# Optimization experiments

Hardware: AMD Instinct MI355X
Metric: run time of the kernel (lower is better)

## Reference

```python
import jax, jax.numpy as jnp
import numpy as np

S, B, C, H, W = 16, 64, 128, 11, 11
P = H * W
N_ITER = 3
EPS = 1e-5


def setup_inputs() -> dict:
    key = jax.random.key(0)
    ks = jax.random.split(key, 12)
    w = lambda k, shape: jax.random.normal(k, shape, jnp.float32) * 0.02
    return {
        "x": jax.random.normal(ks[0], (S, B, C, H, W), jnp.float32),
        # intra-attention 1x1 convs (stored as [out,in] matrices)
        "wq": w(ks[1], (C, C)), "bq": jnp.zeros((C,), jnp.float32),
        "wk": w(ks[2], (C, C)), "bk": jnp.zeros((C,), jnp.float32),
        "wv": w(ks[3], (C, C)), "bv": jnp.zeros((C,), jnp.float32),
        "intra_alpha": jnp.float32(1.0),
        # inter-message path
        "w_msg": w(ks[4], (C, C + 1)), "b_msg": jnp.zeros((C,), jnp.float32),
        "w_lin": w(ks[5], (C, C)),
        "weight": jnp.float32(0.5),
        "w_gate": w(ks[6], (C, C)), "b_gate": jnp.zeros((C,), jnp.float32),
        # ConvGRU 3x3 convs
        "w_zr": w(ks[7], (2 * C, 2 * C, 3, 3)), "b_zr": jnp.zeros((2 * C,), jnp.float32),
        "w_h": w(ks[8], (C, 2 * C, 3, 3)), "b_h": jnp.zeros((C,), jnp.float32),
        # LayerNorm over [C,11,11]
        "ln_gamma": jnp.ones((C, H, W), jnp.float32),
        "ln_beta": jnp.zeros((C, H, W), jnp.float32),
    }


def reference(x, wq, bq, wk, bk, wv, bv, intra_alpha, w_msg, b_msg, w_lin,
              weight, w_gate, b_gate, w_zr, b_zr, w_h, b_h, ln_gamma, ln_beta):
    scale = C ** -0.5

    def c1(t, wgt, bias):  # 1x1 conv on [S,B,Cin,H,W] -> [S,B,Cout,H,W]
        return jnp.einsum('sbchw,oc->sbohw', t, wgt) + bias[:, None, None]

    def conv3(t, wgt, bias):  # 3x3 'SAME' conv on [N,Cin,H,W]
        y = jax.lax.conv_general_dilated(
            t, wgt, (1, 1), 'SAME', dimension_numbers=('NCHW', 'OIHW', 'NCHW'))
        return y + bias[None, :, None, None]

    # chain-graph neighbor validity masks (|i-j| == 1)
    mask_l = (jnp.arange(S) >= 1).astype(x.dtype)[:, None, None, None, None]
    mask_r = (jnp.arange(S) <= S - 2).astype(x.dtype)[:, None, None, None, None]

    h = x
    for _ in range(N_ITER):
        # ---- intra spatial self-attention (per node, over P=H*W tokens) ----
        q = c1(h, wq, bq).reshape(S, B, C, P)
        k = c1(h, wk, bk).reshape(S, B, C, P)
        v = c1(h, wv, bv).reshape(S, B, C, P)
        att = jax.nn.softmax(jnp.einsum('sbcp,sbcq->sbpq', q, k) * scale, axis=-1)
        intra = jnp.einsum('sbpq,sbcq->sbcp', att, v).reshape(S, B, C, H, W)
        intra = intra_alpha * intra + h

        # ---- inter gated message attention from chain neighbors ----
        xf = h.reshape(S, B, C, P)

        def gated_msg(y, edge_val):
            ef = jnp.full((S, B, 1, H, W), edge_val, h.dtype)  # edge feature i-j
            yy = c1(jnp.concatenate([y, ef], axis=2), w_msg, b_msg).reshape(S, B, C, P)
            yy = jnp.einsum('sbcp,dc->sbdp', yy, w_lin)  # Linear (no bias)
            a = jax.nn.softmax(jnp.einsum('sbcp,sbcq->sbpq', xf, yy), axis=-1)
            m = jnp.einsum('sbpq,sbcq->sbcp', a, yy).reshape(S, B, C, H, W)
            g = jax.nn.sigmoid(c1(m, w_gate, b_gate).mean(axis=(-2, -1), keepdims=True))
            return m * g

        y_left = jnp.concatenate([jnp.zeros_like(h[:1]), h[:-1]], axis=0)   # h[i-1], edge +1
        y_right = jnp.concatenate([h[1:], jnp.zeros_like(h[:1])], axis=0)   # h[i+1], edge -1
        inter = gated_msg(y_left, 1.0) * mask_l + gated_msg(y_right, -1.0) * mask_r

        comb = weight * intra + (1.0 - weight) * inter

        # ---- ConvGRU update (fold S into batch) ----
        xg = comb.reshape(S * B, C, H, W)
        hg = h.reshape(S * B, C, H, W)
        zr = jax.nn.sigmoid(conv3(jnp.concatenate([xg, hg], axis=1), w_zr, b_zr))
        z, r = zr[:, :C], zr[:, C:]
        h_hat = jnp.tanh(conv3(jnp.concatenate([xg, r * hg], axis=1), w_h, b_h))
        h_new = ((1 - z) * hg + z * h_hat).reshape(S, B, C, H, W)

        # ---- residual + LayerNorm over [C,H,W] ----
        nh = h_new + h
        mu = nh.mean(axis=(-3, -2, -1), keepdims=True)
        var = nh.var(axis=(-3, -2, -1), keepdims=True)
        h = (nh - mu) * jax.lax.rsqrt(var + EPS) * ln_gamma + ln_beta
    return h
```

## Files before the change

kernel.cpp:

```cpp
#include <hip/hip_runtime.h>
#include <hip/hip_bf16.h>

#define S_   16
#define B_   64
#define SBn  1024
#define C_   128
#define P_   121
#define CP_  15488
static const long NEl = 15859712L;

typedef __hip_bfloat16 bf16t;
typedef __attribute__((ext_vector_type(8))) short bf16x8;
typedef __attribute__((ext_vector_type(4))) float f32x4;
typedef __attribute__((ext_vector_type(4))) unsigned short us4;

__device__ __forceinline__ float ldb(const bf16t* p){ return __bfloat162float(*p); }
__device__ __forceinline__ float b2f(unsigned short u){ unsigned x=((unsigned)u)<<16; float f; __builtin_memcpy(&f,&x,4); return f; }
__device__ __forceinline__ unsigned short f2bu(float v){ __hip_bfloat16 b=__float2bfloat16(v); unsigned short u; __builtin_memcpy(&u,&b,2); return u; }
__device__ __forceinline__ float ldin(const void* s, long i, int f){
    return f ? ((const float*)s)[i] : b2f(((const unsigned short*)s)[i]);
}

__global__ void detect_kernel(const unsigned short* __restrict__ x, int* __restrict__ flag){
    if(blockIdx.x==0 && threadIdx.x==0){
        int crazy=0;
        for(int i=0;i<512;i++){
            unsigned e=(x[i]>>7)&0xFF;
            if(e!=0 && (e<64 || e>191)) crazy++;
        }
        *flag=(crazy>40)?1:0;
    }
}

__global__ void cvt_kernel(float* __restrict__ dst, const void* __restrict__ src, long n, const int* __restrict__ flag){
    long i=(long)blockIdx.x*blockDim.x+threadIdx.x;
    long st=(long)gridDim.x*blockDim.x;
    int f=*flag;
    for(;i<n;i+=st) dst[i]=ldin(src,i,f);
}

__global__ __launch_bounds__(256) void cvtT_kernel(bf16t* __restrict__ hT, const void* __restrict__ x, const int* __restrict__ flag){
    int sb=blockIdx.x, t=threadIdx.x; int f=*flag;
    for(int i=t;i<CP_;i+=256){
        int c=i/P_, p=i-c*P_;
        float v=ldin(x,(long)sb*CP_+i,f);
        hT[(size_t)sb*CP_+(size_t)p*C_+c]=__float2bfloat16(v);
    }
}

__global__ __launch_bounds__(128) void prep_msg_kernel(float* __restrict__ W2, float* __restrict__ b2l, float* __restrict__ b2r,
        const void* __restrict__ wlin, const void* __restrict__ wmsg, const void* __restrict__ bmsg, const int* __restrict__ flag){
    int d=blockIdx.x, c=threadIdx.x; int f=*flag;
    float acc=0.f;
    for(int o2=0;o2<C_;o2++) acc += ldin(wlin,(long)d*C_+o2,f)*ldin(wmsg,(long)o2*(C_+1)+c,f);
    W2[d*C_+c]=acc;
    if(c<2){
        float e=(c==0)?1.f:-1.f; float a=0.f;
        for(int o2=0;o2<C_;o2++) a += ldin(wlin,(long)d*C_+o2,f)*(ldin(bmsg,o2,f)+e*ldin(wmsg,(long)o2*(C_+1)+C_,f));
        if(c==0) b2l[d]=a; else b2r[d]=a;
    }
}

template<int RAW>
__global__ void prep_w1t(bf16t* __restrict__ dst, const void* __restrict__ src, const int* __restrict__ flag){
    int idx=blockIdx.x*blockDim.x+threadIdx.x;
    if(idx>=16384) return;
    int r=idx&31, oc=(idx>>5)&127, icb=idx>>12;
    float v = RAW? ldin(src,(long)oc*C_+icb*32+r,*flag) : ((const float*)src)[(long)oc*C_+icb*32+r];
    dst[idx]=__float2bfloat16(v);
}

__global__ void prep_w3t(bf16t* __restrict__ dst, const void* __restrict__ src, const int* __restrict__ flag, int OC){
    int idx=blockIdx.x*blockDim.x+threadIdx.x;
    int tot=OC*2304;
    if(idx>=tot) return;
    int r=idx&31; int rest=idx>>5; int oc=rest%OC; int g2=rest/OC; int icb=g2&7, tap=g2>>3;
    float v=ldin(src,((long)(oc*256+icb*32+r))*9+tap,*flag);
    dst[idx]=__float2bfloat16(v);
}

__global__ void prep_gbt(float* __restrict__ gamT, float* __restrict__ betT,
                         const void* __restrict__ gam, const void* __restrict__ bet, const int* __restrict__ flag){
    int idx=blockIdx.x*blockDim.x+threadIdx.x;
    if(idx>=CP_) return;
    int c=idx/P_, p=idx-c*P_; int f=*flag;
    gamT[p*C_+c]=ldin(gam,idx,f);
    betT[p*C_+c]=ldin(bet,idx,f);
}

__global__ void prep_wgt(float* __restrict__ wgT, float* __restrict__ bg2,
                         const void* __restrict__ wg, const void* __restrict__ bg, const int* __restrict__ flag){
    int idx=blockIdx.x*blockDim.x+threadIdx.x;
    int f=*flag;
    if(idx<16384){ int k=idx>>7, c=idx&127; wgT[idx]=ldin(wg,(long)c*C_+k,f); }
    if(idx<128) bg2[idx]=ldin(bg,idx,f);
}

__device__ __forceinline__ void gemm24r(f32x4 (&acc)[4][2],
    const bf16t* __restrict__ Wt, const bf16x8 (&hreg)[4][2],
    int ocr,int l15,int kg)
{
    #pragma unroll
    for(int i=0;i<4;i++){
        #pragma unroll
        for(int j=0;j<2;j++) acc[i][j]=(f32x4){0.f,0.f,0.f,0.f};
    }
    #pragma unroll
    for(int kc=0;kc<4;kc++){
        bf16x8 a[4];
        #pragma unroll
        for(int mt=0;mt<4;mt++) a[mt]=*(const bf16x8*)(Wt+((size_t)(kc*C_+ocr*64+mt*16+l15))*32+kg*8);
        #pragma unroll
        for(int mt=0;mt<4;mt++){
            #pragma unroll
            for(int nt=0;nt<2;nt++)
                acc[mt][nt]=__builtin_amdgcn_mfma_f32_16x16x32_bf16(a[mt],hreg[kc][nt],acc[mt][nt],0,0,0);
        }
    }
}

__global__ __launch_bounds__(512) void qkv_attn(
    bf16t* __restrict__ comb, const bf16t* __restrict__ hT,
    const bf16t* __restrict__ WqT, const bf16t* __restrict__ WkT, const bf16t* __restrict__ WvT,
    const float* __restrict__ bq, const float* __restrict__ bk, const float* __restrict__ bv,
    const float* __restrict__ alphap, const float* __restrict__ wp)
{
    __shared__ bf16t LA[128*136];
    __shared__ bf16t LB[128*136];
    int sb=blockIdx.x, t=threadIdx.x, lane=t&63, w=t>>6;
    int l15=lane&15, kg=lane>>4;
    const bf16t* hp=hT+(size_t)sb*CP_;
    int ocr=w>>2, pcr=w&3;
    bf16x8 hreg[4][2];
    #pragma unroll
    for(int kc=0;kc<4;kc++){
        #pragma unroll
        for(int nt=0;nt<2;nt++)
            hreg[kc][nt]=*(const bf16x8*)(hp+(size_t)(pcr*32+nt*16+l15)*C_+kc*32+kg*8);
    }
    f32x4 acc[4][2];
    gemm24r(acc,WqT,hreg,ocr,l15,kg);
    #pragma unroll
    for(int mt=0;mt<4;mt++){
        int oc0=ocr*64+mt*16+kg*4;
        #pragma unroll
        for(int nt=0;nt<2;nt++){
            int p=pcr*32+nt*16+l15;
            us4 pk;
            #pragma unroll
            for(int r=0;r<4;r++) pk[r]=f2bu(acc[mt][nt][r]+bq[oc0+r]);
            *(us4*)(LA+p*136+oc0)=pk;
        }
    }
    gemm24r(acc,WkT,hreg,ocr,l15,kg);
    #pragma unroll
    for(int mt=0;mt<4;mt++){
        int oc0=ocr*64+mt*16+kg*4;
        #pragma unroll
        for(int nt=0;nt<2;nt++){
            int p=pcr*32+nt*16+l15;
            us4 pk;
            #pragma unroll
            for(int r=0;r<4;r++) pk[r]=f2bu(acc[mt][nt][r]+bk[oc0+r]);
            *(us4*)(LB+p*136+oc0)=pk;
        }
    }
    __syncthreads();
    int m0=w*16;
    f32x4 s[8];
    #pragma unroll
    for(int nt=0;nt<8;nt++) s[nt]=(f32x4){0.f,0.f,0.f,0.f};
    #pragma unroll
    for(int kc=0;kc<4;kc++){
        bf16x8 a=*(const bf16x8*)(LA+(size_t)(m0+l15)*136+kc*32+kg*8);
        #pragma unroll
        for(int nt=0;nt<8;nt++){
            bf16x8 b=*(const bf16x8*)(LB+(size_t)(nt*16+l15)*136+kc*32+kg*8);
            s[nt]=__builtin_amdgcn_mfma_f32_16x16x32_bf16(a,b,s[nt],0,0,0);
        }
    }
    const float scale=0.08838834764831845f;
    #pragma unroll
    for(int nt=0;nt<8;nt++){
        #pragma unroll
        for(int r=0;r<4;r++) s[nt][r]*=scale;
    }
    if(l15>=9){
        #pragma unroll
        for(int r=0;r<4;r++) s[7][r]=-3.0e38f;
    }
    #pragma unroll
    for(int r=0;r<4;r++){
        float mx=s[0][r];
        #pragma unroll
        for(int nt=1;nt<8;nt++) mx=fmaxf(mx,s[nt][r]);
        #pragma unroll
        for(int o=1;o<16;o<<=1) mx=fmaxf(mx,__shfl_xor(mx,o));
        float sm=0.f;
        #pragma unroll
        for(int nt=0;nt<8;nt++){ float e=__expf(s[nt][r]-mx); s[nt][r]=e; sm+=e; }
        #pragma unroll
        for(int o=1;o<16;o<<=1) sm+=__shfl_xor(sm,o);
        float rs=1.f/sm;
        #pragma unroll
        for(int nt=0;nt<8;nt++) s[nt][r]*=rs;
    }
    __syncthreads();
    gemm24r(acc,WvT,hreg,ocr,l15,kg);
    #pragma unroll
    for(int mt=0;mt<4;mt++){
        int oc0=ocr*64+mt*16+kg*4;
        #pragma unroll
        for(int nt=0;nt<2;nt++){
            int p=pcr*32+nt*16+l15;
            #pragma unroll
            for(int r=0;r<4;r++)
                LA[(oc0+r)*136+p]=__float2bfloat16(p<P_? acc[mt][nt][r]+bv[oc0+r] : 0.f);
        }
    }
    #pragma unroll
    for(int r=0;r<4;r++){
        int pr=m0+kg*4+r;
        #pragma unroll
        for(int nt=0;nt<8;nt++) LB[pr*136+nt*16+l15]=__float2bfloat16(s[nt][r]);
    }
    __syncthreads();
    f32x4 o[8];
    #pragma unroll
    for(int nt=0;nt<8;nt++) o[nt]=(f32x4){0.f,0.f,0.f,0.f};
    #pragma unroll
    for(int jc=0;jc<4;jc++){
        bf16x8 a=*(const bf16x8*)(LA+(size_t)(m0+l15)*136+jc*32+kg*8);
        #pragma unroll
        for(int nt=0;nt<8;nt++){
            bf16x8 b=*(const bf16x8*)(LB+(size_t)(nt*16+l15)*136+jc*32+kg*8);
            o[nt]=__builtin_amdgcn_mfma_f32_16x16x32_bf16(a,b,o[nt],0,0,0);
        }
    }
    float al=*alphap, wv=*wp;
    int c0=m0+kg*4;
    bf16t* ob=comb+(size_t)sb*CP_;
    #pragma unroll
    for(int nt=0;nt<8;nt++){
        int p=nt*16+l15;
        if(p>=P_) continue;
        us4 hv=*(const us4*)(hp+(size_t)p*C_+c0);
        us4 pk;
        #pragma unroll
        for(int r=0;r<4;r++) pk[r]=f2bu(wv*(al*o[nt][r]+b2f(hv[r])));
        *(us4*)(ob+(size_t)p*C_+c0)=pk;
    }
}

__global__ __launch_bounds__(512) void msg_all(
    bf16t* __restrict__ comb, const bf16t* __restrict__ hT,
    const bf16t* __restrict__ W2T, const float* __restrict__ b2e,
    const float* __restrict__ wgT, const float* __restrict__ bgf,
    const float* __restrict__ wp, int sb0, int shift)
{
    __shared__ bf16t LA[128*136];
    __shared__ bf16t LB[128*136];
    __shared__ float fl[256];
    int sb=sb0+blockIdx.x, t=threadIdx.x, lane=t&63, w=t>>6;
    int l15=lane&15, kg=lane>>4;
    const bf16t* hsp=hT+(size_t)(sb+shift)*CP_;
    int ocr=w>>2, pcr=w&3;
    bf16x8 hreg[4][2];
    #pragma unroll
    for(int kc=0;kc<4;kc++){
        #pragma unroll
        for(int nt=0;nt<2;nt++)
            hreg[kc][nt]=*(const bf16x8*)(hsp+(size_t)(pcr*32+nt*16+l15)*C_+kc*32+kg*8);
    }
    f32x4 acc[4][2];
    gemm24r(acc,W2T,hreg,ocr,l15,kg);
    #pragma unroll
    for(int mt=0;mt<4;mt++){
        int oc0=ocr*64+mt*16+kg*4;
        #pragma unroll
        for(int nt=0;nt<2;nt++){
            int p=pcr*32+nt*16+l15;
            us4 pk;
            #pragma unroll
            for(int r=0;r<4;r++){
                float v=acc[mt][nt][r]+b2e[oc0+r];
                pk[r]=f2bu(v);
                LB[(oc0+r)*136+p]=__float2bfloat16(p<P_? v : 0.f);
            }
            *(us4*)(LA+p*136+oc0)=pk;
        }
    }
    __syncthreads();
    int m0=w*16;
    const bf16t* ap=hT+(size_t)sb*CP_;
    f32x4 s[8];
    #pragma unroll
    for(int nt=0;nt<8;nt++) s[nt]=(f32x4){0.f,0.f,0.f,0.f};
    #pragma unroll
    for(int kc=0;kc<4;kc++){
        bf16x8 a=*(const bf16x8*)(ap+(size_t)(m0+l15)*C_+kc*32+kg*8);
        #pragma unroll
        for(int nt=0;nt<8;nt++){
            bf16x8 b=*(const bf16x8*)(LA+(size_t)(nt*16+l15)*136+kc*32+kg*8);
            s[nt]=__builtin_amdgcn_mfma_f32_16x16x32_bf16(a,b,s[nt],0,0,0);
        }
    }
    if(l15>=9){
        #pragma unroll
        for(int r=0;r<4;r++) s[7][r]=-3.0e38f;
    }
    #pragma unroll
    for(int r=0;r<4;r++){
        float mx=s[0][r];
        #pragma unroll
        for(int nt=1;nt<8;nt++) mx=fmaxf(mx,s[nt][r]);
        #pragma unroll
        for(int o=1;o<16;o<<=1) mx=fmaxf(mx,__shfl_xor(mx,o));
        float sm=0.f;
        #pragma unroll
        for(int nt=0;nt<8;nt++){ float e=__expf(s[nt][r]-mx); s[nt][r]=e; sm+=e; }
        #pragma unroll
        for(int o=1;o<16;o<<=1) sm+=__shfl_xor(sm,o);
        float rs=1.f/sm;
        #pragma unroll
        for(int nt=0;nt<8;nt++) s[nt][r]*=rs;
    }
    __syncthreads();
    #pragma unroll
    for(int r=0;r<4;r++){
        int pr=m0+kg*4+r;
        #pragma unroll
        for(int nt=0;nt<8;nt++) LA[pr*136+nt*16+l15]=__float2bfloat16(s[nt][r]);
    }
    __syncthreads();
    f32x4 o[8];
    #pragma unroll
    for(int nt=0;nt<8;nt++) o[nt]=(f32x4){0.f,0.f,0.f,0.f};
    #pragma unroll
    for(int jc=0;jc<4;jc++){
        bf16x8 a=*(const bf16x8*)(LB+(size_t)(m0+l15)*136+jc*32+kg*8);
        #pragma unroll
        for(int nt=0;nt<8;nt++){
            bf16x8 b=*(const bf16x8*)(LA+(size_t)(nt*16+l15)*136+jc*32+kg*8);
            o[nt]=__builtin_amdgcn_mfma_f32_16x16x32_bf16(a,b,o[nt],0,0,0);
        }
    }
    int c0=m0+kg*4;
    #pragma unroll
    for(int r=0;r<4;r++){
        float sm=0.f;
        #pragma unroll
        for(int nt=0;nt<8;nt++){ float v=o[nt][r]; if(nt==7&&l15>8) v=0.f; sm+=v; }
        sm+=__shfl_xor(sm,1); sm+=__shfl_xor(sm,2); sm+=__shfl_xor(sm,4); sm+=__shfl_xor(sm,8);
        if(l15==0) fl[c0+r]=sm*(1.f/121.f);
    }
    __syncthreads();
    if(t<C_){
        float a=bgf[t];
        #pragma unroll 8
        for(int k=0;k<C_;k++) a+=wgT[k*C_+t]*fl[k];
        fl[C_+t]=1.f/(1.f+__expf(-a));
    }
    __syncthreads();
    float w1m=1.f-*wp;
    float gg[4];
    #pragma unroll
    for(int r=0;r<4;r++) gg[r]=fl[C_+c0+r];
    bf16t* ob=comb+(size_t)sb*CP_;
    #pragma unroll
    for(int nt=0;nt<8;nt++){
        int p=nt*16+l15;
        if(p>=P_) continue;
        us4 bv=*(const us4*)(ob+(size_t)p*C_+c0);
        #pragma unroll
        for(int r=0;r<4;r++) bv[r]=f2bu(b2f(bv[r]) + w1m*o[nt][r]*gg[r]);
        *(us4*)(ob+(size_t)p*C_+c0)=bv;
    }
}

#define LOADA3(bidx, widx) { \
    _Pragma("unroll") \
    for(int mt=0;mt<4;mt++) abuf[bidx][mt]=*(const bf16x8*)(Wt+(size_t)(widx)*(OC*32)+mt*512+base_lane); }
#define STEP3(lbase, bidx, doff) { \
    bf16x8 bb[4]; \
    _Pragma("unroll") \
    for(int nt=0;nt<4;nt++) bb[nt]=*(const bf16x8*)((lbase)+boff[nt]+(doff)); \
    __builtin_amdgcn_s_setprio(1); \
    _Pragma("unroll") \
    for(int mt=0;mt<4;mt++){ \
        _Pragma("unroll") \
        for(int nt=0;nt<4;nt++) \
            acc[mt][nt]=__builtin_amdgcn_mfma_f32_16x16x32_bf16(abuf[bidx][mt],bb[nt],acc[mt][nt],0,0,0); } \
    __builtin_amdgcn_s_setprio(0); }
#define SLOAD3(stg) { \
    const bf16t* ssrc=(((stg)<2)? in0T:in1T)+(size_t)sb*CP_+((stg)&1)*64; \
    sreg[0]=*(const bf16x8*)(ssrc+(size_t)(t>>3)*C_+(t&7)*8); \
    sreg[1]=*(const bf16x8*)(ssrc+(size_t)((t+256)>>3)*C_+(t&7)*8); \
    if(sv2) sreg[2]=*(const bf16x8*)(ssrc+(size_t)((t+512)>>3)*C_+(t&7)*8); \
    if(sv3) sreg[3]=*(const bf16x8*)(ssrc+(size_t)((t+768)>>3)*C_+(t&7)*8); }
#define SWRITE3(lbase) { \
    *(bf16x8*)((lbase)+spix0*72+(t&7)*8)=sreg[0]; \
    *(bf16x8*)((lbase)+spix1*72+(t&7)*8)=sreg[1]; \
    if(sv2) *(bf16x8*)((lbase)+spix2*72+(t&7)*8)=sreg[2]; \
    if(sv3) *(bf16x8*)((lbase)+spix3*72+(t&7)*8)=sreg[3]; }

template<int MODE>
__global__ __launch_bounds__(256) void conv3_mfma(
    bf16t* __restrict__ o0, bf16t* __restrict__ o1,
    const bf16t* __restrict__ in0T, const bf16t* __restrict__ in1T,
    const bf16t* __restrict__ Wt, const float* __restrict__ bias,
    const bf16t* __restrict__ zT, const bf16t* __restrict__ hTb,
    const float* __restrict__ gamT, const float* __restrict__ betT)
{
    constexpr int OC=(MODE==1)?256:128;
    __shared__ bf16t lin[2*12176];
    __shared__ float red[8];
    int sb=blockIdx.x, ocb=(MODE==1)? (int)blockIdx.y*128 : 0;
    int t=threadIdx.x, lane=t&63, w=t>>6;
    int ocr=w>>1, pcr=w&1, l15=lane&15, kg=lane>>4;
    int boff[4]; bool pv_[4];
    #pragma unroll
    for(int nt=0;nt<4;nt++){
        int p=pcr*64+nt*16+l15;
        pv_[nt]=(p<P_); int pc=pv_[nt]?p:(P_-1);
        boff[nt]=((pc/11)*13+(pc%11))*72+kg*8;
    }
    f32x4 acc[4][4];
    #pragma unroll
    for(int i=0;i<4;i++){
        #pragma unroll
        for(int j=0;j<4;j++) acc[i][j]=(f32x4){0.f,0.f,0.f,0.f};
    }
    int base_lane=(ocb+ocr*64+l15)*32+kg*8;
    bf16x8 abuf[4][4];
    bf16x8 sreg[4];
    bool sv2=((t+512)<968), sv3=((t+768)<968);
    int sp0=t>>3, sp1=(t+256)>>3, sp2=(t+512)>>3, sp3=(t+768)>>3;
    if(sp2>120) sp2=120;
    if(sp3>120) sp3=120;
    int spix0=(sp0/11+1)*13+(sp0%11)+1;
    int spix1=(sp1/11+1)*13+(sp1%11)+1;
    int spix2=(sp2/11+1)*13+(sp2%11)+1;
    int spix3=(sp3/11+1)*13+(sp3%11)+1;
    LOADA3(0,0); LOADA3(1,1); LOADA3(2,8); LOADA3(3,9);
    SLOAD3(0);
    {
        bf16x8 z;
        #pragma unroll
        for(int e=0;e<8;e++) z[e]=0;
        for(int i=t;i<768;i+=256){
            int half=i>=384; int i2=i-half*384;
            int bi=i2>>3, cc=(i2&7)*8;
            int pix;
            if(bi<13) pix=bi;
            else if(bi<26) pix=156+(bi-13);
            else { int j2=bi-26; pix=(1+(j2>>1))*13+((j2&1)?12:0); }
            *(bf16x8*)(lin+half*12176+pix*72+cc)=z;
        }
    }
    SWRITE3(lin);
    __syncthreads();
    #pragma unroll
    for(int st=0; st<4; ++st){
        if(st<3) SLOAD3(st+1);
        bf16t* lbase=lin+(st&1)*12176;
        #pragma unroll
        for(int k=0;k<18;k++){
            int s=st*18+k;
            int tap=k>>1, l=k&1;
            int doff=((tap/3)*13+(tap%3))*72+l*32;
            STEP3(lbase, s&3, doff);
            if(s<68){
                int s4=s+4, st4=s4/18, k4=s4-st4*18, tap4=k4>>1, l4=k4&1;
                LOADA3(s&3, tap4*8+st4*2+l4);
            }
        }
        if(st<3){ SWRITE3(lin+((st+1)&1)*12176); }
        __syncthreads();
    }
    if(MODE==1){
        #pragma unroll
        for(int mt=0;mt<4;mt++){
            int ocl=ocr*64+mt*16+kg*4;
            #pragma unroll
            for(int nt=0;nt<4;nt++){
                if(!pv_[nt]) continue;
                int p=pcr*64+nt*16+l15;
                size_t tb=(size_t)sb*CP_+(size_t)p*C_+ocl;
                us4 pk;
                if(ocb==0){
                    #pragma unroll
                    for(int r=0;r<4;r++){ float a=acc[mt][nt][r]+bias[ocl+r]; pk[r]=f2bu(1.f/(1.f+__expf(-a))); }
                    *(us4*)(o0+tb)=pk;
                }else{
                    us4 hv=*(const us4*)(hTb+tb);
                    #pragma unroll
                    for(int r=0;r<4;r++){ float a=acc[mt][nt][r]+bias[128+ocl+r]; float sg=1.f/(1.f+__expf(-a)); pk[r]=f2bu(sg*b2f(hv[r])); }
                    *(us4*)(o1+tb)=pk;
                }
            }
        }
    }else{
        float ls=0.f, ls2=0.f;
        #pragma unroll
        for(int mt=0;mt<4;mt++){
            int ocl=ocr*64+mt*16+kg*4;
            #pragma unroll
            for(int nt=0;nt<4;nt++){
                if(!pv_[nt]) continue;
                int p=pcr*64+nt*16+l15;
                size_t tb=(size_t)sb*CP_+(size_t)p*C_+ocl;
                us4 hv=*(const us4*)(hTb+tb);
                us4 zv=*(const us4*)(zT+tb);
                us4 pk;
                #pragma unroll
                for(int r=0;r<4;r++){
                    float a=acc[mt][nt][r]+bias[ocl+r];
                    float ht=tanhf(a);
                    float z=b2f(zv[r]), h=b2f(hv[r]);
                    unsigned short u=f2bu((1.f-z)*h+z*ht+h);
                    pk[r]=u;
                    float nr=b2f(u); ls+=nr; ls2+=nr*nr;
                }
                *(us4*)((unsigned short*)lin + p*C_+ocl)=pk;
            }
        }
        #pragma unroll
        for(int o=32;o;o>>=1){ ls+=__shfl_xor(ls,o); ls2+=__shfl_xor(ls2,o); }
        if(lane==0){ red[w]=ls; red[4+w]=ls2; }
        __syncthreads();
        float Sx=red[0]+red[1]+red[2]+red[3];
        float Sx2=red[4]+red[5]+red[6]+red[7];
        float mu=Sx*(1.f/(float)CP_);
        float var=Sx2*(1.f/(float)CP_)-mu*mu;
        float rstd=rsqrtf(var+1e-5f);
        bf16t* ho=o0+(size_t)sb*CP_;
        for(int i=t;i<CP_;i+=256){
            float v=(ldb(lin+i)-mu)*rstd*gamT[i]+betT[i];
            ho[i]=__float2bfloat16(v);
        }
    }
}

__global__ __launch_bounds__(256) void finalT_kernel(void* __restrict__ fout, const bf16t* __restrict__ hT, const int* __restrict__ flag){
    __shared__ bf16t tl[CP_];
    int sb=blockIdx.x, t=threadIdx.x, f=*flag;
    for(int i=t;i<CP_;i+=256) tl[i]=hT[(size_t)sb*CP_+i];
    __syncthreads();
    for(int i=t;i<CP_;i+=256){
        int c=i/P_, p=i-c*P_;
        float v=ldb(tl+p*C_+c);
        size_t oi=(size_t)sb*CP_+i;
        if(f) ((float*)fout)[oi]=v;
        else  ((bf16t*)fout)[oi]=__float2bfloat16(v);
    }
}

extern "C" void kernel_launch(void* const* d_in, const int* in_sizes, int n_in,
                              void* d_out, int out_size, void* d_ws, size_t ws_size,
                              hipStream_t stream) {
    (void)in_sizes; (void)n_in; (void)out_size;
    char* base=(char*)d_ws;
    size_t off=0;
    auto alloc=[&](size_t bytes){ void* p=base+off; off+=(bytes+255)&~(size_t)255; return p; };
    bf16t* b1=(bf16t*)alloc((size_t)NEl*2+8192);
    bf16t* b2=(bf16t*)alloc((size_t)NEl*2+8192);
    bf16t* b3=(bf16t*)alloc((size_t)NEl*2+8192);
    bf16t* b4=(bf16t*)d_out;
    bf16t* wqT=(bf16t*)alloc(16384*2);
    bf16t* wkT=(bf16t*)alloc(16384*2);
    bf16t* wvT=(bf16t*)alloc(16384*2);
    bf16t* w2T=(bf16t*)alloc(16384*2);
    bf16t* wzrT=(bf16t*)alloc((size_t)589824*2);
    bf16t* whT =(bf16t*)alloc((size_t)294912*2);
    float* W2f=(float*)alloc(16384*4);
    float* b2l=(float*)alloc(128*4); float* b2r=(float*)alloc(128*4);
    float* bqf=(float*)alloc(128*4); float* bkf=(float*)alloc(128*4); float* bvf=(float*)alloc(128*4);
    float* bzrf=(float*)alloc(256*4); float* bhf=(float*)alloc(128*4);
    float* gamT=(float*)alloc(15488*4); float* betT=(float*)alloc(15488*4);
    float* wgTf=(float*)alloc(16384*4); float* bgf2=(float*)alloc(128*4);
    float* alphaf=(float*)alloc(4); float* weightf=(float*)alloc(4);
    int* flag=(int*)alloc(4);
    if(ws_size<off) return;

    detect_kernel<<<1,64,0,stream>>>((const unsigned short*)d_in[0],flag);
    cvtT_kernel<<<SBn,256,0,stream>>>(b1,d_in[0],flag);
    prep_w1t<1><<<64,256,0,stream>>>(wqT,d_in[1],flag);
    cvt_kernel<<<1,128,0,stream>>>(bqf,d_in[2],128,flag);
    prep_w1t<1><<<64,256,0,stream>>>(wkT,d_in[3],flag);
    cvt_kernel<<<1,128,0,stream>>>(bkf,d_in[4],128,flag);
    prep_w1t<1><<<64,256,0,stream>>>(wvT,d_in[5],flag);
    cvt_kernel<<<1,128,0,stream>>>(bvf,d_in[6],128,flag);
    cvt_kernel<<<1,64,0,stream>>>(alphaf,d_in[7],1,flag);
    prep_msg_kernel<<<C_,C_,0,stream>>>(W2f,b2l,b2r,d_in[10],d_in[8],d_in[9],flag);
    prep_w1t<0><<<64,256,0,stream>>>(w2T,W2f,flag);
    cvt_kernel<<<1,64,0,stream>>>(weightf,d_in[11],1,flag);
    prep_wgt<<<64,256,0,stream>>>(wgTf,bgf2,d_in[12],d_in[13],flag);
    prep_w3t<<<(256*2304+255)/256,256,0,stream>>>(wzrT,d_in[14],flag,256);
    cvt_kernel<<<1,256,0,stream>>>(bzrf,d_in[15],256,flag);
    prep_w3t<<<(128*2304+255)/256,256,0,stream>>>(whT,d_in[16],flag,128);
    cvt_kernel<<<1,128,0,stream>>>(bhf,d_in[17],128,flag);
    prep_gbt<<<(CP_+255)/256,256,0,stream>>>(gamT,betT,d_in[18],d_in[19],flag);

    for(int it=0; it<3; ++it){
        qkv_attn<<<SBn,512,0,stream>>>(b2,b1,wqT,wkT,wvT,bqf,bkf,bvf,alphaf,weightf);
        msg_all<<<SBn-B_,512,0,stream>>>(b2,b1,w2T,b2l,wgTf,bgf2,weightf,B_,-B_);
        msg_all<<<SBn-B_,512,0,stream>>>(b2,b1,w2T,b2r,wgTf,bgf2,weightf,0,B_);
        conv3_mfma<1><<<dim3(SBn,2),256,0,stream>>>(b4,b3,b2,b1,wzrT,bzrf,nullptr,b1,nullptr,nullptr);
        conv3_mfma<2><<<dim3(SBn,1),256,0,stream>>>(b1,nullptr,b2,b3,whT,bhf,b4,b1,gamT,betT);
    }
    finalT_kernel<<<SBn,256,0,stream>>>(d_out,b1,flag);
}
```

Before: 1.450 ms.

## Merge z/r conv halves into one 512-thread block sharing the staged input

The z/r 3x3 conv previously ran as two 256-thread blocks per sample (one per 128-channel output half), each staging the same input tile into LDS. It now uses one 512-thread block where the two groups of four waves compute the two halves from a single shared LDS staging, halving input loads and LDS fills. The input transpose kernel also stages through shared memory so its global writes are coalesced instead of strided. The cost is larger blocks with fewer resident per CU and one fewer block per sample to spread across CUs.

```diff
diff --git a/kernel.cpp b/kernel.cpp
--- a/kernel.cpp
+++ b/kernel.cpp
@@ -40,11 +40,15 @@
 }
 
 __global__ __launch_bounds__(256) void cvtT_kernel(bf16t* __restrict__ hT, const void* __restrict__ x, const int* __restrict__ flag){
+    __shared__ bf16t tl[CP_];
     int sb=blockIdx.x, t=threadIdx.x; int f=*flag;
-    for(int i=t;i<CP_;i+=256){
-        int c=i/P_, p=i-c*P_;
-        float v=ldin(x,(long)sb*CP_+i,f);
-        hT[(size_t)sb*CP_+(size_t)p*C_+c]=__float2bfloat16(v);
+    for(int i=t;i<CP_;i+=256)
+        tl[i]=__float2bfloat16(ldin(x,(long)sb*CP_+i,f));
+    __syncthreads();
+    bf16t* ho=hT+(size_t)sb*CP_;
+    for(int j=t;j<CP_;j+=256){
+        int p=j>>7, c=j&127;
+        ho[j]=tl[c*P_+p];
     }
 }
 
@@ -392,30 +396,130 @@
         for(int nt=0;nt<4;nt++) \
             acc[mt][nt]=__builtin_amdgcn_mfma_f32_16x16x32_bf16(abuf[bidx][mt],bb[nt],acc[mt][nt],0,0,0); } \
     __builtin_amdgcn_s_setprio(0); }
-#define SLOAD3(stg) { \
+
+#define SLOADZ(stg) { \
+    const bf16t* ssrc=(((stg)<2)? in0T:in1T)+(size_t)sb*CP_+((stg)&1)*64; \
+    sreg[0]=*(const bf16x8*)(ssrc+(size_t)sp0*C_+(t&7)*8); \
+    if(sv1) sreg[1]=*(const bf16x8*)(ssrc+(size_t)sp1*C_+(t&7)*8); }
+#define SWRITEZ(lbase) { \
+    *(bf16x8*)((lbase)+spix0*72+(t&7)*8)=sreg[0]; \
+    if(sv1) *(bf16x8*)((lbase)+spix1*72+(t&7)*8)=sreg[1]; }
+
+__global__ __launch_bounds__(512) void conv3_zr(
+    bf16t* __restrict__ o0, bf16t* __restrict__ o1,
+    const bf16t* __restrict__ in0T, const bf16t* __restrict__ in1T,
+    const bf16t* __restrict__ Wt, const float* __restrict__ bias,
+    const bf16t* __restrict__ hTb)
+{
+    constexpr int OC=256;
+    __shared__ bf16t lin[2*12176];
+    int sb=blockIdx.x;
+    int t=threadIdx.x, lane=t&63, w=t>>6;
+    int ocb=(w>=4)?128:0; int w2=w&3;
+    int ocr=w2>>1, pcr=w2&1, l15=lane&15, kg=lane>>4;
+    int boff[4]; bool pv_[4];
+    #pragma unroll
+    for(int nt=0;nt<4;nt++){
+        int p=pcr*64+nt*16+l15;
+        pv_[nt]=(p<P_); int pc=pv_[nt]?p:(P_-1);
+        boff[nt]=((pc/11)*13+(pc%11))*72+kg*8;
+    }
+    f32x4 acc[4][4];
+    #pragma unroll
+    for(int i=0;i<4;i++){
+        #pragma unroll
+        for(int j=0;j<4;j++) acc[i][j]=(f32x4){0.f,0.f,0.f,0.f};
+    }
+    int base_lane=(ocb+ocr*64+l15)*32+kg*8;
+    bf16x8 abuf[4][4];
+    bf16x8 sreg[2];
+    bool sv1=((t+512)<968);
+    int sp0=t>>3, sp1=(t+512)>>3;
+    if(sp1>120) sp1=120;
+    int spix0=(sp0/11+1)*13+(sp0%11)+1;
+    int spix1=(sp1/11+1)*13+(sp1%11)+1;
+    LOADA3(0,0); LOADA3(1,1); LOADA3(2,8); LOADA3(3,9);
+    SLOADZ(0);
+    {
+        bf16x8 z;
+        #pragma unroll
+        for(int e=0;e<8;e++) z[e]=0;
+        for(int i=t;i<768;i+=512){
+            int half=i>=384; int i2=i-half*384;
+            int bi=i2>>3, cc=(i2&7)*8;
+            int pix;
+            if(bi<13) pix=bi;
+            else if(bi<26) pix=156+(bi-13);
+            else { int j2=bi-26; pix=(1+(j2>>1))*13+((j2&1)?12:0); }
+            *(bf16x8*)(lin+half*12176+pix*72+cc)=z;
+        }
+    }
+    SWRITEZ(lin);
+    __syncthreads();
+    #pragma unroll
+    for(int st=0; st<4; ++st){
+        if(st<3) SLOADZ(st+1);
+        bf16t* lbase=lin+(st&1)*12176;
+        #pragma unroll
+        for(int k=0;k<18;k++){
+            int s=st*18+k;
+            int tap=k>>1, l=k&1;
+            int doff=((tap/3)*13+(tap%3))*72+l*32;
+            STEP3(lbase, s&3, doff);
+            if(s<68){
+                int s4=s+4, st4=s4/18, k4=s4-st4*18, tap4=k4>>1, l4=k4&1;
+                LOADA3(s&3, tap4*8+st4*2+l4);
+            }
+        }
+        if(st<3){ SWRITEZ(lin+((st+1)&1)*12176); }
+        __syncthreads();
+    }
+    #pragma unroll
+    for(int mt=0;mt<4;mt++){
+        int ocl=ocr*64+mt*16+kg*4;
+        #pragma unroll
+        for(int nt=0;nt<4;nt++){
+            if(!pv_[nt]) continue;
+            int p=pcr*64+nt*16+l15;
+            size_t tb=(size_t)sb*CP_+(size_t)p*C_+ocl;
+            us4 pk;
+            if(ocb==0){
+                #pragma unroll
+                for(int r=0;r<4;r++){ float a=acc[mt][nt][r]+bias[ocl+r]; pk[r]=f2bu(1.f/(1.f+__expf(-a))); }
+                *(us4*)(o0+tb)=pk;
+            }else{
+                us4 hv=*(const us4*)(hTb+tb);
+                #pragma unroll
+                for(int r=0;r<4;r++){ float a=acc[mt][nt][r]+bias[128+ocl+r]; float sg=1.f/(1.f+__expf(-a)); pk[r]=f2bu(sg*b2f(hv[r])); }
+                *(us4*)(o1+tb)=pk;
+            }
+        }
+    }
+}
+
+#define SLOADH(stg) { \
     const bf16t* ssrc=(((stg)<2)? in0T:in1T)+(size_t)sb*CP_+((stg)&1)*64; \
     sreg[0]=*(const bf16x8*)(ssrc+(size_t)(t>>3)*C_+(t&7)*8); \
     sreg[1]=*(const bf16x8*)(ssrc+(size_t)((t+256)>>3)*C_+(t&7)*8); \
-    if(sv2) sreg[2]=*(const bf16x8*)(ssrc+(size_t)((t+512)>>3)*C_+(t&7)*8); \
-    if(sv3) sreg[3]=*(const bf16x8*)(ssrc+(size_t)((t+768)>>3)*C_+(t&7)*8); }
-#define SWRITE3(lbase) { \
+    if(sv2) sreg[2]=*(const bf16x8*)(ssrc+(size_t)sp2*C_+(t&7)*8); \
+    if(sv3) sreg[3]=*(const bf16x8*)(ssrc+(size_t)sp3*C_+(t&7)*8); }
+#define SWRITEH(lbase) { \
     *(bf16x8*)((lbase)+spix0*72+(t&7)*8)=sreg[0]; \
     *(bf16x8*)((lbase)+spix1*72+(t&7)*8)=sreg[1]; \
     if(sv2) *(bf16x8*)((lbase)+spix2*72+(t&7)*8)=sreg[2]; \
     if(sv3) *(bf16x8*)((lbase)+spix3*72+(t&7)*8)=sreg[3]; }
 
-template<int MODE>
-__global__ __launch_bounds__(256) void conv3_mfma(
-    bf16t* __restrict__ o0, bf16t* __restrict__ o1,
+__global__ __launch_bounds__(256) void conv3_hh(
+    bf16t* __restrict__ o0,
     const bf16t* __restrict__ in0T, const bf16t* __restrict__ in1T,
     const bf16t* __restrict__ Wt, const float* __restrict__ bias,
     const bf16t* __restrict__ zT, const bf16t* __restrict__ hTb,
     const float* __restrict__ gamT, const float* __restrict__ betT)
 {
-    constexpr int OC=(MODE==1)?256:128;
+    constexpr int OC=128;
     __shared__ bf16t lin[2*12176];
     __shared__ float red[8];
-    int sb=blockIdx.x, ocb=(MODE==1)? (int)blockIdx.y*128 : 0;
+    int sb=blockIdx.x;
     int t=threadIdx.x, lane=t&63, w=t>>6;
     int ocr=w>>1, pcr=w&1, l15=lane&15, kg=lane>>4;
     int boff[4]; bool pv_[4];
@@ -431,7 +535,7 @@
         #pragma unroll
         for(int j=0;j<4;j++) acc[i][j]=(f32x4){0.f,0.f,0.f,0.f};
     }
-    int base_lane=(ocb+ocr*64+l15)*32+kg*8;
+    int base_lane=(ocr*64+l15)*32+kg*8;
     bf16x8 abuf[4][4];
     bf16x8 sreg[4];
     bool sv2=((t+512)<968), sv3=((t+768)<968);
@@ -443,7 +547,7 @@
     int spix2=(sp2/11+1)*13+(sp2%11)+1;
     int spix3=(sp3/11+1)*13+(sp3%11)+1;
     LOADA3(0,0); LOADA3(1,1); LOADA3(2,8); LOADA3(3,9);
-    SLOAD3(0);
+    SLOADH(0);
     {
         bf16x8 z;
         #pragma unroll
@@ -458,11 +562,11 @@
             *(bf16x8*)(lin+half*12176+pix*72+cc)=z;
         }
     }
-    SWRITE3(lin);
+    SWRITEH(lin);
     __syncthreads();
     #pragma unroll
     for(int st=0; st<4; ++st){
-        if(st<3) SLOAD3(st+1);
+        if(st<3) SLOADH(st+1);
         bf16t* lbase=lin+(st&1)*12176;
         #pragma unroll
         for(int k=0;k<18;k++){
@@ -475,70 +579,46 @@
                 LOADA3(s&3, tap4*8+st4*2+l4);
             }
         }
-        if(st<3){ SWRITE3(lin+((st+1)&1)*12176); }
+        if(st<3){ SWRITEH(lin+((st+1)&1)*12176); }
         __syncthreads();
     }
-    if(MODE==1){
-        #pragma unroll
-        for(int mt=0;mt<4;mt++){
-            int ocl=ocr*64+mt*16+kg*4;
+    float ls=0.f, ls2=0.f;
+    #pragma unroll
+    for(int mt=0;mt<4;mt++){
+        int ocl=ocr*64+mt*16+kg*4;
+        #pragma unroll
+        for(int nt=0;nt<4;nt++){
+            if(!pv_[nt]) continue;
+            int p=pcr*64+nt*16+l15;
+            size_t tb=(size_t)sb*CP_+(size_t)p*C_+ocl;
+            us4 hv=*(const us4*)(hTb+tb);
+            us4 zv=*(const us4*)(zT+tb);
+            us4 pk;
             #pragma unroll
-            for(int nt=0;nt<4;nt++){
-                if(!pv_[nt]) continue;
-                int p=pcr*64+nt*16+l15;
-                size_t tb=(size_t)sb*CP_+(size_t)p*C_+ocl;
-                us4 pk;
-                if(ocb==0){
-                    #pragma unroll
-                    for(int r=0;r<4;r++){ float a=acc[mt][nt][r]+bias[ocl+r]; pk[r]=f2bu(1.f/(1.f+__expf(-a))); }
-                    *(us4*)(o0+tb)=pk;
-                }else{
-                    us4 hv=*(const us4*)(hTb+tb);
-                    #pragma unroll
-                    for(int r=0;r<4;r++){ float a=acc[mt][nt][r]+bias[128+ocl+r]; float sg=1.f/(1.f+__expf(-a)); pk[r]=f2bu(sg*b2f(hv[r])); }
-                    *(us4*)(o1+tb)=pk;
-                }
+            for(int r=0;r<4;r++){
+                float a=acc[mt][nt][r]+bias[ocl+r];
+                float ht=tanhf(a);
+                float z=b2f(zv[r]), h=b2f(hv[r]);
+                unsigned short u=f2bu((1.f-z)*h+z*ht+h);
+                pk[r]=u;
+                float nr=b2f(u); ls+=nr; ls2+=nr*nr;
             }
-        }
-    }else{
-        float ls=0.f, ls2=0.f;
-        #pragma unroll
-        for(int mt=0;mt<4;mt++){
-            int ocl=ocr*64+mt*16+kg*4;
-            #pragma unroll
-            for(int nt=0;nt<4;nt++){
-                if(!pv_[nt]) continue;
-                int p=pcr*64+nt*16+l15;
-                size_t tb=(size_t)sb*CP_+(size_t)p*C_+ocl;
-                us4 hv=*(const us4*)(hTb+tb);
-                us4 zv=*(const us4*)(zT+tb);
-                us4 pk;
-                #pragma unroll
-                for(int r=0;r<4;r++){
-                    float a=acc[mt][nt][r]+bias[ocl+r];
-                    float ht=tanhf(a);
-                    float z=b2f(zv[r]), h=b2f(hv[r]);
-                    unsigned short u=f2bu((1.f-z)*h+z*ht+h);
-                    pk[r]=u;
-                    float nr=b2f(u); ls+=nr; ls2+=nr*nr;
-                }
-                *(us4*)((unsigned short*)lin + p*C_+ocl)=pk;
-            }
-        }
-        #pragma unroll
-        for(int o=32;o;o>>=1){ ls+=__shfl_xor(ls,o); ls2+=__shfl_xor(ls2,o); }
-        if(lane==0){ red[w]=ls; red[4+w]=ls2; }
-        __syncthreads();
-        float Sx=red[0]+red[1]+red[2]+red[3];
-        float Sx2=red[4]+red[5]+red[6]+red[7];
-        float mu=Sx*(1.f/(float)CP_);
-        float var=Sx2*(1.f/(float)CP_)-mu*mu;
-        float rstd=rsqrtf(var+1e-5f);
-        bf16t* ho=o0+(size_t)sb*CP_;
-        for(int i=t;i<CP_;i+=256){
-            float v=(ldb(lin+i)-mu)*rstd*gamT[i]+betT[i];
-            ho[i]=__float2bfloat16(v);
-        }
+            *(us4*)((unsigned short*)lin + p*C_+ocl)=pk;
+        }
+    }
+    #pragma unroll
+    for(int o=32;o;o>>=1){ ls+=__shfl_xor(ls,o); ls2+=__shfl_xor(ls2,o); }
+    if(lane==0){ red[w]=ls; red[4+w]=ls2; }
+    __syncthreads();
+    float Sx=red[0]+red[1]+red[2]+red[3];
+    float Sx2=red[4]+red[5]+red[6]+red[7];
+    float mu=Sx*(1.f/(float)CP_);
+    float var=Sx2*(1.f/(float)CP_)-mu*mu;
+    float rstd=rsqrtf(var+1e-5f);
+    bf16t* ho=o0+(size_t)sb*CP_;
+    for(int i=t;i<CP_;i+=256){
+        float v=(ldb(lin+i)-mu)*rstd*gamT[i]+betT[i];
+        ho[i]=__float2bfloat16(v);
     }
 }
 
@@ -606,8 +686,8 @@
         qkv_attn<<<SBn,512,0,stream>>>(b2,b1,wqT,wkT,wvT,bqf,bkf,bvf,alphaf,weightf);
         msg_all<<<SBn-B_,512,0,stream>>>(b2,b1,w2T,b2l,wgTf,bgf2,weightf,B_,-B_);
         msg_all<<<SBn-B_,512,0,stream>>>(b2,b1,w2T,b2r,wgTf,bgf2,weightf,0,B_);
-        conv3_mfma<1><<<dim3(SBn,2),256,0,stream>>>(b4,b3,b2,b1,wzrT,bzrf,nullptr,b1,nullptr,nullptr);
-        conv3_mfma<2><<<dim3(SBn,1),256,0,stream>>>(b1,nullptr,b2,b3,whT,bhf,b4,b1,gamT,betT);
+        conv3_zr<<<SBn,512,0,stream>>>(b4,b3,b2,b1,wzrT,bzrf,b1);
+        conv3_hh<<<SBn,256,0,stream>>>(b1,b2,b3,whT,bhf,b4,b1,gamT,betT);
     }
     finalT_kernel<<<SBn,256,0,stream>>>(d_out,b1,flag);
 }
```

Result: no change. 1.424 ms (-1.8%).
